# Kernel optimization log

Hardware: AMD Instinct MI355X
Metric: run time of the kernel (lower is better)

## Reference

```python
import jax, jax.numpy as jnp
import numpy as np

N_NODES = 100000


def setup_inputs() -> dict:
    key = jax.random.key(0)
    k1, k2, k3, k4, k5, k6 = jax.random.split(key, 6)
    n_edges = 1600000
    in_f, out_f = 64, 64
    x = jax.random.normal(k1, (N_NODES, in_f), dtype=jnp.float32)
    edge_row = jax.random.randint(k2, (n_edges,), 0, N_NODES, dtype=jnp.int32)
    edge_col = jax.random.randint(k3, (n_edges,), 0, N_NODES, dtype=jnp.int32)
    edge_val = jax.random.uniform(k4, (n_edges,), dtype=jnp.float32)
    stdv = 1.0 / np.sqrt(out_f)
    weight = jax.random.uniform(k5, (in_f, out_f), dtype=jnp.float32, minval=-stdv, maxval=stdv)
    bias = jax.random.uniform(k6, (out_f,), dtype=jnp.float32, minval=-stdv, maxval=stdv)
    return {"x": x, "edge_row": edge_row, "edge_col": edge_col,
            "edge_val": edge_val, "weight": weight, "bias": bias}


def reference(x, edge_row, edge_col, edge_val, weight, bias):
    # spmm: support[i] = sum_{e: row[e]==i} val[e] * x[col[e]]
    msgs = edge_val[:, None] * x[edge_col]              # [E, in_f]
    support = jax.ops.segment_sum(msgs, edge_row, num_segments=N_NODES)  # [N, in_f]
    out = support @ weight + bias                       # [N, out_f]
    # row-wise L2 normalize (no eps, matching torch.norm division)
    norm = jnp.linalg.norm(out, axis=1, keepdims=True)  # [N, 1]
    return out / norm
```

## Files before the change

### kernel.cpp

```cpp
#include <hip/hip_runtime.h>

#define N_NODES 100000
#define FDIM 64
#define BROWS 128
#define NBUCK ((N_NODES + BROWS - 1) / BROWS)
#define EDGES_PER_BLK 8192
#define BCAP 3072

#define WS_BBASE_OFF (656u * 1024u)
#define WS_BTOT_OFF  (672u * 1024u)
#define WS_CV_OFF    (1024u * 1024u)
#define WS_XH_OFF    (14u * 1024u * 1024u)

__global__ __launch_bounds__(256) void spmm_atomic(
    const float* __restrict__ x, const int* __restrict__ erow,
    const int* __restrict__ ecol, const float* __restrict__ eval,
    float* __restrict__ out, int n_edges)
{
    int tid = blockIdx.x * 256 + threadIdx.x;
    int e = tid >> 4, l = tid & 15;
    if (e >= n_edges) return;
    int row = erow[e], col = ecol[e];
    float v = eval[e];
    const float4 xv = *reinterpret_cast<const float4*>(x + (size_t)col * FDIM + l * 4);
    float* dst = out + (size_t)row * FDIM + l * 4;
    unsafeAtomicAdd(dst + 0, v * xv.x);
    unsafeAtomicAdd(dst + 1, v * xv.y);
    unsafeAtomicAdd(dst + 2, v * xv.z);
    unsafeAtomicAdd(dst + 3, v * xv.w);
}

__global__ __launch_bounds__(256) void convert_x(
    const float* __restrict__ x, unsigned short* __restrict__ xh)
{
    const int i = (blockIdx.x * 256 + threadIdx.x) * 8;
    const float4 a = *reinterpret_cast<const float4*>(x + i);
    const float4 b = *reinterpret_cast<const float4*>(x + i + 4);
    ushort4 ha, hb;
    #define BF16RNE(f) ((unsigned short)(((__float_as_uint(f) + 0x7FFFu + ((__float_as_uint(f) >> 16) & 1u)) >> 16)))
    ha.x = BF16RNE(a.x); ha.y = BF16RNE(a.y); ha.z = BF16RNE(a.z); ha.w = BF16RNE(a.w);
    hb.x = BF16RNE(b.x); hb.y = BF16RNE(b.y); hb.z = BF16RNE(b.z); hb.w = BF16RNE(b.w);
    #undef BF16RNE
    *reinterpret_cast<ushort4*>(xh + i)     = ha;
    *reinterpret_cast<ushort4*>(xh + i + 4) = hb;
}

__global__ __launch_bounds__(1024) void count_blocks(
    const int* __restrict__ erow, int* __restrict__ cnts,
    int n_edges, int nblk)
{
    __shared__ int cnt[NBUCK];
    const int blk = blockIdx.x, t = threadIdx.x;
    for (int i = t; i < NBUCK; i += 1024) cnt[i] = 0;
    __syncthreads();
    const int beg = blk * EDGES_PER_BLK;
    const int end = min(beg + EDGES_PER_BLK, n_edges);
    for (int i = beg + t; i < end; i += 1024)
        atomicAdd(&cnt[erow[i] >> 7], 1);
    __syncthreads();
    for (int b = t; b < NBUCK; b += 1024)
        cnts[b * nblk + blk] = cnt[b];
}

__global__ __launch_bounds__(256) void scan_within_bucket(
    int* __restrict__ cnts, int* __restrict__ btot, int nblk)
{
    __shared__ int ssum[256];
    const int b = blockIdx.x, t = threadIdx.x;
    const int c = (t < nblk) ? cnts[b * nblk + t] : 0;
    ssum[t] = c;
    __syncthreads();
    for (int off = 1; off < 256; off <<= 1) {
        int v = (t >= off) ? ssum[t - off] : 0;
        __syncthreads();
        ssum[t] += v;
        __syncthreads();
    }
    if (t < nblk) cnts[b * nblk + t] = ssum[t] - c;
    if (t == 255) btot[b] = ssum[255];
}

__global__ __launch_bounds__(1024) void scan_btot(
    const int* __restrict__ btot, int* __restrict__ bbase, int n_edges)
{
    __shared__ int ssum[1024];
    const int t = threadIdx.x;
    const int v0 = (t < NBUCK) ? btot[t] : 0;
    ssum[t] = v0;
    __syncthreads();
    for (int off = 1; off < 1024; off <<= 1) {
        int v = (t >= off) ? ssum[t - off] : 0;
        __syncthreads();
        ssum[t] += v;
        __syncthreads();
    }
    if (t < NBUCK) bbase[t] = ssum[t] - v0;
    if (t == 0) bbase[NBUCK] = n_edges;
}

__global__ __launch_bounds__(1024) void bin_pass2(
    const int* __restrict__ erow, const int* __restrict__ ecol,
    const float* __restrict__ eval, const int* __restrict__ cnts,
    const int* __restrict__ bbase, int2* __restrict__ cvbin,
    int n_edges, int nblk)
{
    __shared__ int cur[NBUCK];
    const int blk = blockIdx.x, t = threadIdx.x;
    for (int b = t; b < NBUCK; b += 1024)
        cur[b] = bbase[b] + cnts[b * nblk + blk];
    __syncthreads();
    const int beg = blk * EDGES_PER_BLK;
    const int end = min(beg + EDGES_PER_BLK, n_edges);
    for (int i = beg + t; i < end; i += 1024) {
        int r = erow[i];
        int b = r >> 7;
        int pos = atomicAdd(&cur[b], 1);
        cvbin[pos] = make_int2(ecol[i] | ((r & 127) << 20), __float_as_int(eval[i]));
    }
}

__global__ __launch_bounds__(256) void sort_bucket(
    const int* __restrict__ bbase, int2* __restrict__ cvbin,
    int* __restrict__ endoff)
{
    __shared__ int2 se[BCAP];
    __shared__ int  hcnt[BROWS];
    __shared__ int  tmp[BROWS];
    __shared__ int  hoff[BROWS];
    const int b = blockIdx.x, t = threadIdx.x;
    const int beg = bbase[b];
    const int end = bbase[b + 1];
    const int n = end - beg;

    for (int i = t; i < n; i += 256) se[i] = cvbin[beg + i];
    if (t < BROWS) hcnt[t] = 0;
    __syncthreads();

    for (int i = t; i < n; i += 256) atomicAdd(&hcnt[se[i].x >> 20], 1);
    __syncthreads();

    if (t < BROWS) tmp[t] = hcnt[t];
    __syncthreads();
    for (int off = 1; off < BROWS; off <<= 1) {
        int val = (t < BROWS && t >= off) ? tmp[t - off] : 0;
        __syncthreads();
        if (t < BROWS) tmp[t] += val;
        __syncthreads();
    }
    if (t < BROWS) hoff[t] = tmp[t] - hcnt[t];
    __syncthreads();

    for (int i = t; i < n; i += 256) {
        int2 e = se[i];
        int pos = atomicAdd(&hoff[e.x >> 20], 1);
        cvbin[beg + pos] = e;
    }
    __syncthreads();

    if (t < BROWS) {
        int row = b * BROWS + t;
        if (row < N_NODES) endoff[row] = beg + hoff[t];
    }
}

__global__ __launch_bounds__(256) void spmm_csr(
    const float* __restrict__ x, const int* __restrict__ endoff,
    const int2* __restrict__ cv, float* __restrict__ out)
{
    const int wave = (blockIdx.x * 256 + threadIdx.x) >> 6;
    if (wave >= N_NODES) return;
    const int lane = threadIdx.x & 63;
    const int sub = lane >> 4, l = lane & 15;
    const int r = wave;
    const int beg = (r == 0) ? 0 : endoff[r - 1];
    const int end = endoff[r];

    float4 acc = {0.f, 0.f, 0.f, 0.f};
    int it = beg + sub;
    for (; it + 12 < end; it += 16) {
        const int2 ea = cv[it];
        const int2 eb = cv[it + 4];
        const int2 ec = cv[it + 8];
        const int2 ed = cv[it + 12];
        const float4 xa = *reinterpret_cast<const float4*>(x + (size_t)(ea.x & 0xFFFFF) * FDIM + l * 4);
        const float4 xb = *reinterpret_cast<const float4*>(x + (size_t)(eb.x & 0xFFFFF) * FDIM + l * 4);
        const float4 xc = *reinterpret_cast<const float4*>(x + (size_t)(ec.x & 0xFFFFF) * FDIM + l * 4);
        const float4 xd = *reinterpret_cast<const float4*>(x + (size_t)(ed.x & 0xFFFFF) * FDIM + l * 4);
        const float va = __int_as_float(ea.y);
        const float vb = __int_as_float(eb.y);
        const float vc = __int_as_float(ec.y);
        const float vd = __int_as_float(ed.y);
        acc.x += va * xa.x; acc.y += va * xa.y; acc.z += va * xa.z; acc.w += va * xa.w;
        acc.x += vb * xb.x; acc.y += vb * xb.y; acc.z += vb * xb.z; acc.w += vb * xb.w;
        acc.x += vc * xc.x; acc.y += vc * xc.y; acc.z += vc * xc.z; acc.w += vc * xc.w;
        acc.x += vd * xd.x; acc.y += vd * xd.y; acc.z += vd * xd.z; acc.w += vd * xd.w;
    }
    for (; it < end; it += 4) {
        const int2 e = cv[it];
        const float v = __int_as_float(e.y);
        const float4 xv = *reinterpret_cast<const float4*>(x + (size_t)(e.x & 0xFFFFF) * FDIM + l * 4);
        acc.x += v * xv.x; acc.y += v * xv.y; acc.z += v * xv.z; acc.w += v * xv.w;
    }
    #pragma unroll
    for (int off = 16; off < 64; off <<= 1) {
        acc.x += __shfl_xor(acc.x, off);
        acc.y += __shfl_xor(acc.y, off);
        acc.z += __shfl_xor(acc.z, off);
        acc.w += __shfl_xor(acc.w, off);
    }
    if (sub == 0)
        *reinterpret_cast<float4*>(out + (size_t)r * FDIM + l * 4) = acc;
}

__device__ __forceinline__ float bf2f(unsigned short h) {
    return __uint_as_float((unsigned int)h << 16);
}

__global__ __launch_bounds__(256) void spmm_csr_h(
    const unsigned short* __restrict__ xh, const int* __restrict__ endoff,
    const int2* __restrict__ cv, float* __restrict__ out)
{
    const int sg = (blockIdx.x * 256 + threadIdx.x) >> 4;
    if (sg >= N_NODES) return;
    const int l = threadIdx.x & 15;
    const int r = sg;
    const int beg = (r == 0) ? 0 : endoff[r - 1];
    const int end = endoff[r];

    float4 acc = {0.f, 0.f, 0.f, 0.f};
    int it = beg;
    for (; it + 3 < end; it += 4) {
        const int2 ea = cv[it];
        const int2 eb = cv[it + 1];
        const int2 ec = cv[it + 2];
        const int2 ed = cv[it + 3];
        const ushort4 xa = *reinterpret_cast<const ushort4*>(xh + (size_t)(ea.x & 0xFFFFF) * FDIM + l * 4);
        const ushort4 xb = *reinterpret_cast<const ushort4*>(xh + (size_t)(eb.x & 0xFFFFF) * FDIM + l * 4);
        const ushort4 xc = *reinterpret_cast<const ushort4*>(xh + (size_t)(ec.x & 0xFFFFF) * FDIM + l * 4);
        const ushort4 xd = *reinterpret_cast<const ushort4*>(xh + (size_t)(ed.x & 0xFFFFF) * FDIM + l * 4);
        const float va = __int_as_float(ea.y);
        const float vb = __int_as_float(eb.y);
        const float vc = __int_as_float(ec.y);
        const float vd = __int_as_float(ed.y);
        acc.x += va * bf2f(xa.x); acc.y += va * bf2f(xa.y); acc.z += va * bf2f(xa.z); acc.w += va * bf2f(xa.w);
        acc.x += vb * bf2f(xb.x); acc.y += vb * bf2f(xb.y); acc.z += vb * bf2f(xb.z); acc.w += vb * bf2f(xb.w);
        acc.x += vc * bf2f(xc.x); acc.y += vc * bf2f(xc.y); acc.z += vc * bf2f(xc.z); acc.w += vc * bf2f(xc.w);
        acc.x += vd * bf2f(xd.x); acc.y += vd * bf2f(xd.y); acc.z += vd * bf2f(xd.z); acc.w += vd * bf2f(xd.w);
    }
    for (; it < end; ++it) {
        const int2 e = cv[it];
        const float v = __int_as_float(e.y);
        const ushort4 xv = *reinterpret_cast<const ushort4*>(xh + (size_t)(e.x & 0xFFFFF) * FDIM + l * 4);
        acc.x += v * bf2f(xv.x); acc.y += v * bf2f(xv.y); acc.z += v * bf2f(xv.z); acc.w += v * bf2f(xv.w);
    }

    *reinterpret_cast<float4*>(out + (size_t)r * FDIM + l * 4) = acc;
}

__global__ __launch_bounds__(256) void gemm_norm(
    float* __restrict__ io, const float* __restrict__ W,
    const float* __restrict__ bias)
{
    __shared__ float4 Wl[64][16];
    __shared__ float4 bl[16];
    __shared__ float  s[4][4][68];

    const int t = threadIdx.x;
    for (int i = t; i < 64 * 16; i += 256)
        ((float4*)Wl)[i] = ((const float4*)W)[i];
    if (t < 16) bl[t] = ((const float4*)bias)[t];

    const int wid  = t >> 6;
    const int lane = t & 63;
    const int sub  = lane >> 4;
    const int l    = lane & 15;
    const long base = (long)blockIdx.x * 16 + wid * 4;

    float4 sv = *reinterpret_cast<const float4*>(io + base * FDIM + lane * 4);
    *reinterpret_cast<float4*>(&s[wid][lane >> 4][(lane & 15) * 4]) = sv;
    __syncthreads();

    float4 acc = {0.f, 0.f, 0.f, 0.f};
    const float* srow = s[wid][sub];
    #pragma unroll
    for (int k = 0; k < FDIM; ++k) {
        const float a = srow[k];
        const float4 w = Wl[k][l];
        acc.x += a * w.x; acc.y += a * w.y; acc.z += a * w.z; acc.w += a * w.w;
    }
    const float4 b = bl[l];
    acc.x += b.x; acc.y += b.y; acc.z += b.z; acc.w += b.w;

    float p = acc.x*acc.x + acc.y*acc.y + acc.z*acc.z + acc.w*acc.w;
    #pragma unroll
    for (int off = 1; off < 16; off <<= 1)
        p += __shfl_xor(p, off);
    const float inv = 1.0f / sqrtf(p);
    acc.x *= inv; acc.y *= inv; acc.z *= inv; acc.w *= inv;

    *reinterpret_cast<float4*>(io + (base + sub) * FDIM + l * 4) = acc;
}

extern "C" void kernel_launch(void* const* d_in, const int* in_sizes, int n_in,
                              void* d_out, int out_size, void* d_ws, size_t ws_size,
                              hipStream_t stream) {
    const float* x    = (const float*)d_in[0];
    const int*   erow = (const int*)d_in[1];
    const int*   ecol = (const int*)d_in[2];
    const float* eval = (const float*)d_in[3];
    const float* W    = (const float*)d_in[4];
    const float* bias = (const float*)d_in[5];
    float* out = (float*)d_out;
    const int n_edges = in_sizes[1];

    const int nblk = (n_edges + EDGES_PER_BLK - 1) / EDGES_PER_BLK;
    const size_t need = (size_t)WS_CV_OFF + (size_t)n_edges * sizeof(int2);
    const size_t need_bf16 = (size_t)WS_XH_OFF + (size_t)N_NODES * FDIM * sizeof(short);
    const bool cnts_fit =
        (size_t)NBUCK * nblk * sizeof(int) <= WS_BBASE_OFF && nblk <= 256;

    if (ws_size >= need && cnts_fit) {
        int*  cnts   = (int*)d_ws;
        int*  endoff = (int*)d_ws;
        int*  bbase  = (int*)((char*)d_ws + WS_BBASE_OFF);
        int*  btot   = (int*)((char*)d_ws + WS_BTOT_OFF);
        int2* cvbin  = (int2*)((char*)d_ws + WS_CV_OFF);
        unsigned short* xh = (unsigned short*)((char*)d_ws + WS_XH_OFF);
        const bool use_bf16 = (ws_size >= need_bf16);

        if (use_bf16)
            convert_x<<<(N_NODES * FDIM) / (256 * 8), 256, 0, stream>>>(x, xh);
        count_blocks<<<nblk, 1024, 0, stream>>>(erow, cnts, n_edges, nblk);
        scan_within_bucket<<<NBUCK, 256, 0, stream>>>(cnts, btot, nblk);
        scan_btot<<<1, 1024, 0, stream>>>(btot, bbase, n_edges);
        bin_pass2<<<nblk, 1024, 0, stream>>>(erow, ecol, eval, cnts, bbase, cvbin,
                                             n_edges, nblk);
        sort_bucket<<<NBUCK, 256, 0, stream>>>(bbase, cvbin, endoff);
        if (use_bf16)
            spmm_csr_h<<<((N_NODES * 16) + 255) / 256, 256, 0, stream>>>(xh, endoff, cvbin, out);
        else
            spmm_csr<<<(N_NODES + 3) / 4, 256, 0, stream>>>(x, endoff, cvbin, out);
    } else {
        hipMemsetAsync(out, 0, (size_t)N_NODES * FDIM * sizeof(float), stream);
        long threads = (long)n_edges * 16;
        spmm_atomic<<<(int)((threads + 255) / 256), 256, 0, stream>>>(
            x, erow, ecol, eval, out, n_edges);
    }

    gemm_norm<<<N_NODES / 16, 256, 0, stream>>>(out, W, bias);
}
```

Measured before the change: 111.0 us.

## Reassociate GEMM before SpMM and fuse bias plus L2 norm into SpMM

```diff
diff --git a/kernel.cpp b/kernel.cpp
--- a/kernel.cpp
+++ b/kernel.cpp
@@ -11,6 +11,14 @@
 #define WS_BTOT_OFF  (672u * 1024u)
 #define WS_CV_OFF    (1024u * 1024u)
 #define WS_XH_OFF    (14u * 1024u * 1024u)
+
+__device__ __forceinline__ unsigned short f2bf(float f) {
+    unsigned int u = __float_as_uint(f);
+    return (unsigned short)((u + 0x7FFFu + ((u >> 16) & 1u)) >> 16);
+}
+__device__ __forceinline__ float bf2f(unsigned short h) {
+    return __uint_as_float((unsigned int)h << 16);
+}
 
 __global__ __launch_bounds__(256) void spmm_atomic(
     const float* __restrict__ x, const int* __restrict__ erow,
@@ -30,19 +38,38 @@
     unsafeAtomicAdd(dst + 3, v * xv.w);
 }
 
-__global__ __launch_bounds__(256) void convert_x(
-    const float* __restrict__ x, unsigned short* __restrict__ xh)
-{
-    const int i = (blockIdx.x * 256 + threadIdx.x) * 8;
-    const float4 a = *reinterpret_cast<const float4*>(x + i);
-    const float4 b = *reinterpret_cast<const float4*>(x + i + 4);
-    ushort4 ha, hb;
-    #define BF16RNE(f) ((unsigned short)(((__float_as_uint(f) + 0x7FFFu + ((__float_as_uint(f) >> 16) & 1u)) >> 16)))
-    ha.x = BF16RNE(a.x); ha.y = BF16RNE(a.y); ha.z = BF16RNE(a.z); ha.w = BF16RNE(a.w);
-    hb.x = BF16RNE(b.x); hb.y = BF16RNE(b.y); hb.z = BF16RNE(b.z); hb.w = BF16RNE(b.w);
-    #undef BF16RNE
-    *reinterpret_cast<ushort4*>(xh + i)     = ha;
-    *reinterpret_cast<ushort4*>(xh + i + 4) = hb;
+__global__ __launch_bounds__(256) void gemm_xw(
+    const float* __restrict__ x, const float* __restrict__ W,
+    unsigned short* __restrict__ yh)
+{
+    __shared__ float4 Wl[64][16];
+    __shared__ float  s[4][4][68];
+
+    const int t = threadIdx.x;
+    for (int i = t; i < 64 * 16; i += 256)
+        ((float4*)Wl)[i] = ((const float4*)W)[i];
+
+    const int wid  = t >> 6;
+    const int lane = t & 63;
+    const int sub  = lane >> 4;
+    const int l    = lane & 15;
+    const long base = (long)blockIdx.x * 16 + wid * 4;
+
+    float4 sv = *reinterpret_cast<const float4*>(x + base * FDIM + lane * 4);
+    *reinterpret_cast<float4*>(&s[wid][lane >> 4][(lane & 15) * 4]) = sv;
+    __syncthreads();
+
+    float4 acc = {0.f, 0.f, 0.f, 0.f};
+    const float* srow = s[wid][sub];
+    #pragma unroll
+    for (int k = 0; k < FDIM; ++k) {
+        const float a = srow[k];
+        const float4 w = Wl[k][l];
+        acc.x += a * w.x; acc.y += a * w.y; acc.z += a * w.z; acc.w += a * w.w;
+    }
+    ushort4 h;
+    h.x = f2bf(acc.x); h.y = f2bf(acc.y); h.z = f2bf(acc.z); h.w = f2bf(acc.w);
+    *reinterpret_cast<ushort4*>(yh + (size_t)(base + sub) * FDIM + l * 4) = h;
 }
 
 __global__ __launch_bounds__(1024) void count_blocks(
@@ -212,20 +239,16 @@
         *reinterpret_cast<float4*>(out + (size_t)r * FDIM + l * 4) = acc;
 }
 
-__device__ __forceinline__ float bf2f(unsigned short h) {
-    return __uint_as_float((unsigned int)h << 16);
-}
-
-__global__ __launch_bounds__(256) void spmm_csr_h(
-    const unsigned short* __restrict__ xh, const int* __restrict__ endoff,
-    const int2* __restrict__ cv, float* __restrict__ out)
+__global__ __launch_bounds__(256) void spmm_fused(
+    const unsigned short* __restrict__ yh, const int* __restrict__ endoff,
+    const int2* __restrict__ cv, const float* __restrict__ bias,
+    float* __restrict__ out)
 {
     const int sg = (blockIdx.x * 256 + threadIdx.x) >> 4;
     if (sg >= N_NODES) return;
     const int l = threadIdx.x & 15;
-    const int r = sg;
-    const int beg = (r == 0) ? 0 : endoff[r - 1];
-    const int end = endoff[r];
+    const int beg = (sg == 0) ? 0 : endoff[sg - 1];
+    const int end = endoff[sg];
 
     float4 acc = {0.f, 0.f, 0.f, 0.f};
     int it = beg;
@@ -234,10 +257,10 @@
         const int2 eb = cv[it + 1];
         const int2 ec = cv[it + 2];
         const int2 ed = cv[it + 3];
-        const ushort4 xa = *reinterpret_cast<const ushort4*>(xh + (size_t)(ea.x & 0xFFFFF) * FDIM + l * 4);
-        const ushort4 xb = *reinterpret_cast<const ushort4*>(xh + (size_t)(eb.x & 0xFFFFF) * FDIM + l * 4);
-        const ushort4 xc = *reinterpret_cast<const ushort4*>(xh + (size_t)(ec.x & 0xFFFFF) * FDIM + l * 4);
-        const ushort4 xd = *reinterpret_cast<const ushort4*>(xh + (size_t)(ed.x & 0xFFFFF) * FDIM + l * 4);
+        const ushort4 xa = *reinterpret_cast<const ushort4*>(yh + (size_t)(ea.x & 0xFFFFF) * FDIM + l * 4);
+        const ushort4 xb = *reinterpret_cast<const ushort4*>(yh + (size_t)(eb.x & 0xFFFFF) * FDIM + l * 4);
+        const ushort4 xc = *reinterpret_cast<const ushort4*>(yh + (size_t)(ec.x & 0xFFFFF) * FDIM + l * 4);
+        const ushort4 xd = *reinterpret_cast<const ushort4*>(yh + (size_t)(ed.x & 0xFFFFF) * FDIM + l * 4);
         const float va = __int_as_float(ea.y);
         const float vb = __int_as_float(eb.y);
         const float vc = __int_as_float(ec.y);
@@ -250,11 +273,21 @@
     for (; it < end; ++it) {
         const int2 e = cv[it];
         const float v = __int_as_float(e.y);
-        const ushort4 xv = *reinterpret_cast<const ushort4*>(xh + (size_t)(e.x & 0xFFFFF) * FDIM + l * 4);
+        const ushort4 xv = *reinterpret_cast<const ushort4*>(yh + (size_t)(e.x & 0xFFFFF) * FDIM + l * 4);
         acc.x += v * bf2f(xv.x); acc.y += v * bf2f(xv.y); acc.z += v * bf2f(xv.z); acc.w += v * bf2f(xv.w);
     }
 
-    *reinterpret_cast<float4*>(out + (size_t)r * FDIM + l * 4) = acc;
+    const float4 b = *reinterpret_cast<const float4*>(bias + l * 4);
+    acc.x += b.x; acc.y += b.y; acc.z += b.z; acc.w += b.w;
+
+    float p = acc.x * acc.x + acc.y * acc.y + acc.z * acc.z + acc.w * acc.w;
+    #pragma unroll
+    for (int off = 1; off < 16; off <<= 1)
+        p += __shfl_xor(p, off);
+    const float inv = 1.0f / sqrtf(p);
+    acc.x *= inv; acc.y *= inv; acc.z *= inv; acc.w *= inv;
+
+    *reinterpret_cast<float4*>(out + (size_t)sg * FDIM + l * 4) = acc;
 }
 
 __global__ __launch_bounds__(256) void gemm_norm(
@@ -325,27 +358,29 @@
         int*  bbase  = (int*)((char*)d_ws + WS_BBASE_OFF);
         int*  btot   = (int*)((char*)d_ws + WS_BTOT_OFF);
         int2* cvbin  = (int2*)((char*)d_ws + WS_CV_OFF);
-        unsigned short* xh = (unsigned short*)((char*)d_ws + WS_XH_OFF);
+        unsigned short* yh = (unsigned short*)((char*)d_ws + WS_XH_OFF);
         const bool use_bf16 = (ws_size >= need_bf16);
 
         if (use_bf16)
-            convert_x<<<(N_NODES * FDIM) / (256 * 8), 256, 0, stream>>>(x, xh);
+            gemm_xw<<<N_NODES / 16, 256, 0, stream>>>(x, W, yh);
         count_blocks<<<nblk, 1024, 0, stream>>>(erow, cnts, n_edges, nblk);
         scan_within_bucket<<<NBUCK, 256, 0, stream>>>(cnts, btot, nblk);
         scan_btot<<<1, 1024, 0, stream>>>(btot, bbase, n_edges);
         bin_pass2<<<nblk, 1024, 0, stream>>>(erow, ecol, eval, cnts, bbase, cvbin,
                                              n_edges, nblk);
         sort_bucket<<<NBUCK, 256, 0, stream>>>(bbase, cvbin, endoff);
-        if (use_bf16)
-            spmm_csr_h<<<((N_NODES * 16) + 255) / 256, 256, 0, stream>>>(xh, endoff, cvbin, out);
-        else
+        if (use_bf16) {
+            spmm_fused<<<((N_NODES * 16) + 255) / 256, 256, 0, stream>>>(
+                yh, endoff, cvbin, bias, out);
+        } else {
             spmm_csr<<<(N_NODES + 3) / 4, 256, 0, stream>>>(x, endoff, cvbin, out);
+            gemm_norm<<<N_NODES / 16, 256, 0, stream>>>(out, W, bias);
+        }
     } else {
         hipMemsetAsync(out, 0, (size_t)N_NODES * FDIM * sizeof(float), stream);
         long threads = (long)n_edges * 16;
         spmm_atomic<<<(int)((threads + 255) / 256), 256, 0, stream>>>(
             x, erow, ecol, eval, out, n_edges);
-    }
-
-    gemm_norm<<<N_NODES / 16, 256, 0, stream>>>(out, W, bias);
-}
+        gemm_norm<<<N_NODES / 16, 256, 0, stream>>>(out, W, bias);
+    }
+}
```

Measured after the change: 102.7 us. -7.5%, faster.
